# Kernel tuning notes

Measured on AMD Instinct MI355X. Metric: run time of the kernel, lower is better.

Reference implementation:

```python
import jax, jax.numpy as jnp
import numpy as np

B, D, L = 512, 512, 24

def setup_inputs() -> dict:
    key = jax.random.key(0)
    k1, k2 = jax.random.split(key)
    source = jax.random.normal(k1, (B, D), dtype=jnp.float32)
    s_labels = jax.random.randint(k2, (B, L), 0, 2, dtype=jnp.int32)
    return {"source": source, "s_labels": s_labels}

def reference(source, s_labels):
    margin = 0.0
    squared = False
    # pairwise squared euclidean distances, (B, B)
    diff = source[:, None, :] - source[None, :, :]          # (B, B, D)
    dist = jnp.clip(jnp.sum(diff * diff, axis=-1), 0.0)     # (B, B)
    if not squared:
        zmask = (dist == 0.0).astype(dist.dtype)
        dist = jnp.sqrt(dist + zmask * 1e-16) * (1.0 - zmask)
    # triplet validity mask: labels[i]==labels[j] (share a label) and labels[i]!=labels[k]
    lab = s_labels.astype(jnp.float32)
    sim = (lab @ lab.T > 0).astype(jnp.float32)              # (B, B)
    mask = sim[:, :, None] * (1.0 - sim[:, None, :])         # (B, B, B)
    # euclidean branch: d_ap - (1 - margin) * d_an
    triplet = dist[:, :, None] - (1.0 - margin) * dist[:, None, :]
    triplet = jnp.clip(mask * triplet, 0.0)                  # (B, B, B)
    num_positive = jnp.sum((triplet > 1e-16).astype(jnp.float32))
    return jnp.sum(triplet) / (num_positive + 1e-16)
```

## Files before the change

kernel.cpp:

```cpp
#include <hip/hip_runtime.h>

#define BN 512
#define DD 512
#define LL 24

__global__ void prep_kernel(const float* __restrict__ src, const int* __restrict__ labels,
                            float* __restrict__ norms, unsigned* __restrict__ masks,
                            float* __restrict__ accum) {
    int i = blockIdx.x;
    int lane = threadIdx.x;
    const float4* row = (const float4*)(src + (size_t)i * DD);
    float4 v0 = row[lane];
    float4 v1 = row[lane + 64];
    float s = v0.x*v0.x + v0.y*v0.y + v0.z*v0.z + v0.w*v0.w
            + v1.x*v1.x + v1.y*v1.y + v1.z*v1.z + v1.w*v1.w;
#pragma unroll
    for (int off = 32; off > 0; off >>= 1) s += __shfl_down(s, off);
    int lab = (lane < LL) ? labels[i * LL + lane] : 0;
    unsigned long long b = __ballot(lab != 0);
    if (lane == 0) {
        norms[i] = s;
        masks[i] = (unsigned)(b & 0xFFFFFFull);
        if (i == 0) { accum[0] = 0.0f; ((unsigned*)accum)[1] = 0u; }
    }
}

__device__ __forceinline__ float dist_val(float d2, bool diag) {
    d2 = fmaxf(d2, 0.0f);
    float d = sqrtf(d2);
    return diag ? 0.0f : d;
}

__global__ void dist_kernel(const float* __restrict__ S, const float* __restrict__ norms,
                            float* __restrict__ Dm) {
    __shared__ float As[32][34];
    __shared__ float Bs[32][34];
    int t  = threadIdx.x;
    int tx = t & 15, ty = t >> 4;
    int jb = blockIdx.x * 32;
    int ib = blockIdx.y * 32;
    int lr = t >> 3;
    int lc = (t & 7) * 4;
    float acc00 = 0.f, acc01 = 0.f, acc10 = 0.f, acc11 = 0.f;
    for (int k0 = 0; k0 < DD; k0 += 32) {
        float4 a = *(const float4*)&S[(size_t)(ib + lr) * DD + k0 + lc];
        float4 b = *(const float4*)&S[(size_t)(jb + lr) * DD + k0 + lc];
        As[lc + 0][lr] = a.x; As[lc + 1][lr] = a.y; As[lc + 2][lr] = a.z; As[lc + 3][lr] = a.w;
        Bs[lc + 0][lr] = b.x; Bs[lc + 1][lr] = b.y; Bs[lc + 2][lr] = b.z; Bs[lc + 3][lr] = b.w;
        __syncthreads();
#pragma unroll
        for (int kk = 0; kk < 32; kk++) {
            float2 av = *(const float2*)&As[kk][ty * 2];
            float2 bv = *(const float2*)&Bs[kk][tx * 2];
            acc00 += av.x * bv.x; acc01 += av.x * bv.y;
            acc10 += av.y * bv.x; acc11 += av.y * bv.y;
        }
        __syncthreads();
    }
    int i0 = ib + ty * 2, j0 = jb + tx * 2;
    float ni0 = norms[i0], ni1 = norms[i0 + 1];
    float nj0 = norms[j0], nj1 = norms[j0 + 1];
    Dm[(size_t)i0 * BN + j0]           = dist_val(ni0 + nj0 - 2.f * acc00, i0 == j0);
    Dm[(size_t)i0 * BN + j0 + 1]       = dist_val(ni0 + nj1 - 2.f * acc01, i0 == j0 + 1);
    Dm[(size_t)(i0 + 1) * BN + j0]     = dist_val(ni1 + nj0 - 2.f * acc10, i0 + 1 == j0);
    Dm[(size_t)(i0 + 1) * BN + j0 + 1] = dist_val(ni1 + nj1 - 2.f * acc11, i0 + 1 == j0 + 1);
}

__global__ void triplet_kernel(const float* __restrict__ Dm, const unsigned* __restrict__ masks,
                               float* __restrict__ accum) {
    __shared__ float drow[BN];
    __shared__ float pos[BN];
    __shared__ float neg[BN];
    __shared__ int pcnt, ncnt;
    __shared__ float wsum[4];
    __shared__ unsigned wcnt[4];
    int i = blockIdx.x;
    int t = threadIdx.x;
    if (t == 0) { pcnt = 0; ncnt = 0; }
    float2 dv = ((const float2*)(Dm + (size_t)i * BN))[t];
    drow[2 * t] = dv.x; drow[2 * t + 1] = dv.y;
    __syncthreads();
    unsigned mi = masks[i];
#pragma unroll
    for (int j = t; j < BN; j += 256) {
        float dj = drow[j];
        if (mi & masks[j]) { int p = atomicAdd(&pcnt, 1); pos[p] = dj; }
        else               { int p = atomicAdd(&ncnt, 1); neg[p] = dj; }
    }
    __syncthreads();
    int P = pcnt, N = ncnt;
    float sum = 0.f;
    unsigned cnt = 0;
    for (int p = t; p < P; p += 256) {
        float a = pos[p];
        for (int n = 0; n < N; n++) {
            float v = a - neg[n];
            sum += fmaxf(v, 0.0f);
            cnt += (v > 1e-16f) ? 1u : 0u;
        }
    }
#pragma unroll
    for (int off = 32; off > 0; off >>= 1) {
        sum += __shfl_down(sum, off);
        cnt += __shfl_down(cnt, off);
    }
    if ((t & 63) == 0) { wsum[t >> 6] = sum; wcnt[t >> 6] = cnt; }
    __syncthreads();
    if (t == 0) {
        sum = wsum[0] + wsum[1] + wsum[2] + wsum[3];
        cnt = wcnt[0] + wcnt[1] + wcnt[2] + wcnt[3];
        if (sum != 0.f || cnt != 0u) {
            atomicAdd(&accum[0], sum);
            atomicAdd((unsigned*)&accum[1], cnt);
        }
    }
}

__global__ void finalize_kernel(const float* __restrict__ accum, float* __restrict__ out) {
    if (threadIdx.x == 0) {
        float s = accum[0];
        float c = (float)((const unsigned*)accum)[1];
        out[0] = s / (c + 1e-16f);
    }
}

extern "C" void kernel_launch(void* const* d_in, const int* in_sizes, int n_in,
                              void* d_out, int out_size, void* d_ws, size_t ws_size,
                              hipStream_t stream) {
    const float* src    = (const float*)d_in[0];
    const int*   labels = (const int*)d_in[1];
    float* ws = (float*)d_ws;
    float*    norms = ws;
    unsigned* masks = (unsigned*)(ws + BN);
    float*    Dm    = ws + 2 * BN;
    float*    accum = ws + 2 * BN + (size_t)BN * BN;

    hipLaunchKernelGGL(prep_kernel,     dim3(BN),     dim3(64),  0, stream, src, labels, norms, masks, accum);
    hipLaunchKernelGGL(dist_kernel,     dim3(16, 16), dim3(256), 0, stream, src, norms, Dm);
    hipLaunchKernelGGL(triplet_kernel,  dim3(BN),     dim3(256), 0, stream, Dm, masks, accum);
    hipLaunchKernelGGL(finalize_kernel, dim3(1),      dim3(64),  0, stream, accum, (float*)d_out);
}
```

Baseline: 79.66 us.

## Fuse prep into distance GEMM and finalize into triplet kernel, aggregate atomics

Merges the norm and label-mask prep into the distance kernel, which now computes row norms from the tiles it already loads, and moves mask building to block (0,0). The finalize step moves into the triplet kernel using a last-block-done counter. This cuts four launches to two. It also register-prefetches the next tile in the GEMM loop, vectorises the Dm stores, and replaces per-thread shared atomics in the pos/neg partition with wave-ballot aggregated atomics. One risk is that block (0,0) serially builds all 512 masks, which lengthens that block.

```diff
diff --git a/kernel.cpp b/kernel.cpp
--- a/kernel.cpp
+++ b/kernel.cpp
@@ -3,27 +3,6 @@
 #define BN 512
 #define DD 512
 #define LL 24
-
-__global__ void prep_kernel(const float* __restrict__ src, const int* __restrict__ labels,
-                            float* __restrict__ norms, unsigned* __restrict__ masks,
-                            float* __restrict__ accum) {
-    int i = blockIdx.x;
-    int lane = threadIdx.x;
-    const float4* row = (const float4*)(src + (size_t)i * DD);
-    float4 v0 = row[lane];
-    float4 v1 = row[lane + 64];
-    float s = v0.x*v0.x + v0.y*v0.y + v0.z*v0.z + v0.w*v0.w
-            + v1.x*v1.x + v1.y*v1.y + v1.z*v1.z + v1.w*v1.w;
-#pragma unroll
-    for (int off = 32; off > 0; off >>= 1) s += __shfl_down(s, off);
-    int lab = (lane < LL) ? labels[i * LL + lane] : 0;
-    unsigned long long b = __ballot(lab != 0);
-    if (lane == 0) {
-        norms[i] = s;
-        masks[i] = (unsigned)(b & 0xFFFFFFull);
-        if (i == 0) { accum[0] = 0.0f; ((unsigned*)accum)[1] = 0u; }
-    }
-}
 
 __device__ __forceinline__ float dist_val(float d2, bool diag) {
     d2 = fmaxf(d2, 0.0f);
@@ -31,23 +10,54 @@
     return diag ? 0.0f : d;
 }
 
-__global__ void dist_kernel(const float* __restrict__ S, const float* __restrict__ norms,
-                            float* __restrict__ Dm) {
+
+__global__ __launch_bounds__(256) void dist_prep_kernel(
+    const float* __restrict__ S, const int* __restrict__ labels,
+    unsigned* __restrict__ masks, float* __restrict__ Dm, float* __restrict__ accum)
+{
     __shared__ float As[32][34];
     __shared__ float Bs[32][34];
-    int t  = threadIdx.x;
-    int tx = t & 15, ty = t >> 4;
-    int jb = blockIdx.x * 32;
-    int ib = blockIdx.y * 32;
-    int lr = t >> 3;
-    int lc = (t & 7) * 4;
+    __shared__ float nrmA[32], nrmB[32];
+    const int t  = threadIdx.x;
+    const int tx = t & 15, ty = t >> 4;
+    const int jb = blockIdx.x * 32;
+    const int ib = blockIdx.y * 32;
+    const int lr = t >> 3;
+    const int lc = (t & 7) * 4;
+
+    if (blockIdx.x == 0 && blockIdx.y == 0) {
+        for (int r = t; r < BN; r += 256) {
+            const int* lab = labels + r * LL;
+            unsigned m = 0;
+#pragma unroll
+            for (int l = 0; l < LL; l++) m |= (lab[l] != 0 ? 1u : 0u) << l;
+            masks[r] = m;
+        }
+        if (t == 0) {
+            accum[0] = 0.0f;
+            ((unsigned*)accum)[1] = 0u;
+            ((unsigned*)accum)[2] = 0u;
+        }
+    }
+
+    const float* Ap = S + (size_t)(ib + lr) * DD + lc;
+    const float* Bp = S + (size_t)(jb + lr) * DD + lc;
+    float4 a = *(const float4*)Ap;
+    float4 b = *(const float4*)Bp;
+    float na = 0.f, nb = 0.f;
     float acc00 = 0.f, acc01 = 0.f, acc10 = 0.f, acc11 = 0.f;
+
     for (int k0 = 0; k0 < DD; k0 += 32) {
-        float4 a = *(const float4*)&S[(size_t)(ib + lr) * DD + k0 + lc];
-        float4 b = *(const float4*)&S[(size_t)(jb + lr) * DD + k0 + lc];
-        As[lc + 0][lr] = a.x; As[lc + 1][lr] = a.y; As[lc + 2][lr] = a.z; As[lc + 3][lr] = a.w;
-        Bs[lc + 0][lr] = b.x; Bs[lc + 1][lr] = b.y; Bs[lc + 2][lr] = b.z; Bs[lc + 3][lr] = b.w;
+        As[lc+0][lr]=a.x; As[lc+1][lr]=a.y; As[lc+2][lr]=a.z; As[lc+3][lr]=a.w;
+        Bs[lc+0][lr]=b.x; Bs[lc+1][lr]=b.y; Bs[lc+2][lr]=b.z; Bs[lc+3][lr]=b.w;
+        na += a.x*a.x + a.y*a.y + a.z*a.z + a.w*a.w;
+        nb += b.x*b.x + b.y*b.y + b.z*b.z + b.w*b.w;
         __syncthreads();
+        float4 a1 = make_float4(0.f,0.f,0.f,0.f), b1 = a1;
+        if (k0 + 32 < DD) {
+            a1 = *(const float4*)(Ap + k0 + 32);
+            b1 = *(const float4*)(Bp + k0 + 32);
+        }
 #pragma unroll
         for (int kk = 0; kk < 32; kk++) {
             float2 av = *(const float2*)&As[kk][ty * 2];
@@ -56,39 +66,70 @@
             acc10 += av.y * bv.x; acc11 += av.y * bv.y;
         }
         __syncthreads();
+        a = a1; b = b1;
     }
-    int i0 = ib + ty * 2, j0 = jb + tx * 2;
-    float ni0 = norms[i0], ni1 = norms[i0 + 1];
-    float nj0 = norms[j0], nj1 = norms[j0 + 1];
-    Dm[(size_t)i0 * BN + j0]           = dist_val(ni0 + nj0 - 2.f * acc00, i0 == j0);
-    Dm[(size_t)i0 * BN + j0 + 1]       = dist_val(ni0 + nj1 - 2.f * acc01, i0 == j0 + 1);
-    Dm[(size_t)(i0 + 1) * BN + j0]     = dist_val(ni1 + nj0 - 2.f * acc10, i0 + 1 == j0);
-    Dm[(size_t)(i0 + 1) * BN + j0 + 1] = dist_val(ni1 + nj1 - 2.f * acc11, i0 + 1 == j0 + 1);
+
+    na += __shfl_down(na, 4, 8); na += __shfl_down(na, 2, 8); na += __shfl_down(na, 1, 8);
+    nb += __shfl_down(nb, 4, 8); nb += __shfl_down(nb, 2, 8); nb += __shfl_down(nb, 1, 8);
+    if ((t & 7) == 0) { nrmA[lr] = na; nrmB[lr] = nb; }
+    __syncthreads();
+
+    const int i0 = ib + ty * 2, j0 = jb + tx * 2;
+    const float ni0 = nrmA[ty*2], ni1 = nrmA[ty*2+1];
+    const float nj0 = nrmB[tx*2], nj1 = nrmB[tx*2+1];
+    float2 r0, r1;
+    r0.x = dist_val(ni0 + nj0 - 2.f * acc00, i0     == j0    );
+    r0.y = dist_val(ni0 + nj1 - 2.f * acc01, i0     == j0 + 1);
+    r1.x = dist_val(ni1 + nj0 - 2.f * acc10, i0 + 1 == j0    );
+    r1.y = dist_val(ni1 + nj1 - 2.f * acc11, i0 + 1 == j0 + 1);
+    *(float2*)&Dm[(size_t)i0 * BN + j0]       = r0;
+    *(float2*)&Dm[(size_t)(i0+1) * BN + j0]   = r1;
 }
 
-__global__ void triplet_kernel(const float* __restrict__ Dm, const unsigned* __restrict__ masks,
-                               float* __restrict__ accum) {
-    __shared__ float drow[BN];
+__global__ __launch_bounds__(256) void triplet_final_kernel(
+    const float* __restrict__ Dm, const unsigned* __restrict__ masks,
+    float* __restrict__ accum, float* __restrict__ out)
+{
     __shared__ float pos[BN];
     __shared__ float neg[BN];
     __shared__ int pcnt, ncnt;
     __shared__ float wsum[4];
     __shared__ unsigned wcnt[4];
-    int i = blockIdx.x;
-    int t = threadIdx.x;
+    const int i = blockIdx.x;
+    const int t = threadIdx.x;
+    const int lane = t & 63;
+    const int w = t >> 6;
     if (t == 0) { pcnt = 0; ncnt = 0; }
-    float2 dv = ((const float2*)(Dm + (size_t)i * BN))[t];
-    drow[2 * t] = dv.x; drow[2 * t + 1] = dv.y;
     __syncthreads();
-    unsigned mi = masks[i];
-#pragma unroll
+    const unsigned mi = masks[i];
+    const float* drow = Dm + (size_t)i * BN;
+    const unsigned long long ltmask = (1ull << lane) - 1ull;
+
     for (int j = t; j < BN; j += 256) {
         float dj = drow[j];
-        if (mi & masks[j]) { int p = atomicAdd(&pcnt, 1); pos[p] = dj; }
-        else               { int p = atomicAdd(&ncnt, 1); neg[p] = dj; }
+        bool isp = (mi & masks[j]) != 0u;
+        unsigned long long bal = __ballot(isp);
+        int np = __popcll(bal);
+        if (np > 0) {
+            int ldr = __ffsll((unsigned long long)bal) - 1;
+            int base = 0;
+            if (lane == ldr) base = atomicAdd(&pcnt, np);
+            base = __shfl(base, ldr);
+            if (isp) pos[base + __popcll(bal & ltmask)] = dj;
+        }
+        unsigned long long nbal = ~bal;
+        int nn = 64 - np;
+        if (nn > 0) {
+            int ldr = __ffsll((unsigned long long)nbal) - 1;
+            int base = 0;
+            if (lane == ldr) base = atomicAdd(&ncnt, nn);
+            base = __shfl(base, ldr);
+            if (!isp) neg[base + __popcll(nbal & ltmask)] = dj;
+        }
     }
     __syncthreads();
-    int P = pcnt, N = ncnt;
+
+    const int P = pcnt, N = ncnt;
     float sum = 0.f;
     unsigned cnt = 0;
     for (int p = t; p < P; p += 256) {
@@ -104,23 +145,20 @@
         sum += __shfl_down(sum, off);
         cnt += __shfl_down(cnt, off);
     }
-    if ((t & 63) == 0) { wsum[t >> 6] = sum; wcnt[t >> 6] = cnt; }
+    if (lane == 0) { wsum[w] = sum; wcnt[w] = cnt; }
     __syncthreads();
     if (t == 0) {
         sum = wsum[0] + wsum[1] + wsum[2] + wsum[3];
         cnt = wcnt[0] + wcnt[1] + wcnt[2] + wcnt[3];
-        if (sum != 0.f || cnt != 0u) {
-            atomicAdd(&accum[0], sum);
-            atomicAdd((unsigned*)&accum[1], cnt);
+        atomicAdd(&accum[0], sum);
+        atomicAdd(&((unsigned*)accum)[1], cnt);
+        __threadfence();
+        unsigned old = atomicAdd(&((unsigned*)accum)[2], 1u);
+        if (old == (unsigned)(gridDim.x - 1)) {
+            float s   = atomicAdd(&accum[0], 0.0f);
+            unsigned c = atomicAdd(&((unsigned*)accum)[1], 0u);
+            out[0] = s / ((float)c + 1e-16f);
         }
-    }
-}
-
-__global__ void finalize_kernel(const float* __restrict__ accum, float* __restrict__ out) {
-    if (threadIdx.x == 0) {
-        float s = accum[0];
-        float c = (float)((const unsigned*)accum)[1];
-        out[0] = s / (c + 1e-16f);
     }
 }
 
@@ -130,13 +168,12 @@
     const float* src    = (const float*)d_in[0];
     const int*   labels = (const int*)d_in[1];
     float* ws = (float*)d_ws;
-    float*    norms = ws;
-    unsigned* masks = (unsigned*)(ws + BN);
-    float*    Dm    = ws + 2 * BN;
-    float*    accum = ws + 2 * BN + (size_t)BN * BN;
+    unsigned* masks = (unsigned*)ws;
+    float*    Dm    = ws + BN;
+    float*    accum = ws + BN + (size_t)BN * BN;
 
-    hipLaunchKernelGGL(prep_kernel,     dim3(BN),     dim3(64),  0, stream, src, labels, norms, masks, accum);
-    hipLaunchKernelGGL(dist_kernel,     dim3(16, 16), dim3(256), 0, stream, src, norms, Dm);
-    hipLaunchKernelGGL(triplet_kernel,  dim3(BN),     dim3(256), 0, stream, Dm, masks, accum);
-    hipLaunchKernelGGL(finalize_kernel, dim3(1),      dim3(64),  0, stream, accum, (float*)d_out);
+    hipLaunchKernelGGL(dist_prep_kernel,     dim3(16, 16), dim3(256), 0, stream,
+                       src, labels, masks, Dm, accum);
+    hipLaunchKernelGGL(triplet_final_kernel, dim3(BN),     dim3(256), 0, stream,
+                       Dm, masks, accum, (float*)d_out);
 }
```

After: 90.62 us. 13.8% more time.
